# Kernel optimization log

Hardware: AMD Instinct MI355X
Metric: run time of the kernel (lower is better)

The kernel has to match this reference:

```python
import jax, jax.numpy as jnp
import numpy as np

DICTSIZE = 256
NUMCHAR = 1024
EMB_LEN = 512
KQV_LEN = 512
BATCH = 128


def setup_inputs() -> dict:
    key = jax.random.key(0)
    ks = jax.random.split(key, 7)
    input_tokens = jax.random.randint(ks[0], (BATCH, NUMCHAR), 0, DICTSIZE, dtype=jnp.int32)
    tok_emb = jax.random.normal(ks[1], (DICTSIZE, EMB_LEN), dtype=jnp.float32)
    Wq = jax.random.normal(ks[2], (KQV_LEN, EMB_LEN), dtype=jnp.float32) * (EMB_LEN ** -0.5)
    Wk = jax.random.normal(ks[3], (KQV_LEN, EMB_LEN), dtype=jnp.float32) * (EMB_LEN ** -0.5)
    Wv = jax.random.normal(ks[4], (KQV_LEN, EMB_LEN), dtype=jnp.float32) * (EMB_LEN ** -0.5)
    W_lin = jax.random.normal(ks[5], (DICTSIZE, NUMCHAR * EMB_LEN), dtype=jnp.float32) * ((NUMCHAR * EMB_LEN) ** -0.5)
    b_lin = jax.random.normal(ks[6], (DICTSIZE,), dtype=jnp.float32) * 0.01
    return {"input_tokens": input_tokens, "tok_emb": tok_emb, "Wq": Wq, "Wk": Wk,
            "Wv": Wv, "W_lin": W_lin, "b_lin": b_lin}


def reference(input_tokens, tok_emb, Wq, Wk, Wv, W_lin, b_lin):
    B, N = input_tokens.shape
    emb = tok_emb[input_tokens]                      # [B, N, E]
    q = jnp.einsum('bne,ke->bnk', emb, Wq)           # [B, N, K]
    k = jnp.einsum('bne,ke->bnk', emb, Wk)           # [B, N, K]
    v = jnp.einsum('bne,ke->bnk', emb, Wv)           # computed but unused (matches torch source)
    scores = jnp.einsum('bqk,bmk->bqm', q, k)        # [B, N, N] (no 1/sqrt(d) scaling in source)
    tril = jnp.tril(jnp.ones((N, N), dtype=bool))
    scores = jnp.where(tril, scores, -jnp.inf)
    attn = jax.nn.softmax(scores, axis=-1)           # [B, N, N]
    aff = jnp.einsum('bqm,bme->bqe', attn, emb)      # note: @ input_emb, NOT value
    aff_flat = aff.reshape(B, N * emb.shape[-1])     # [B, N*E]
    outputs = aff_flat @ W_lin.T + b_lin             # [B, dictsize]
    return outputs
```

## Files before the change

### kernel.cpp

```cpp
#include <hip/hip_runtime.h>

typedef _Float16 f16;
typedef _Float16 half8 __attribute__((ext_vector_type(8)));
typedef _Float16 half4 __attribute__((ext_vector_type(4)));
typedef float floatx4 __attribute__((ext_vector_type(4)));
typedef float floatx16 __attribute__((ext_vector_type(16)));

#define MFMA16(A, B, C) __builtin_amdgcn_mfma_f32_16x16x32_f16((A), (B), (C), 0, 0, 0)
#define MFMA32(A, B, C) __builtin_amdgcn_mfma_f32_32x32x16_f16((A), (B), (C), 0, 0, 0)


__global__ __launch_bounds__(256) void k_gemm_M(const float* __restrict__ Wq,
                                                const float* __restrict__ Wk,
                                                f16* __restrict__ Mt) {
  __shared__ __align__(16) float qa[16][64];
  __shared__ __align__(16) float kbs[16][64];
  const int tid = threadIdx.x;
  const int i0 = (blockIdx.x & 7) * 64;
  const int j0 = (blockIdx.x >> 3) * 64;
  const int tx = tid & 15, ty = tid >> 4;
  float acc[4][4] = {};
  for (int k0 = 0; k0 < 512; k0 += 16) {
    __syncthreads();
    const int kr = tid >> 4;
    const int c4 = (tid & 15) * 4;
    *(float4*)&qa[kr][c4]  = *(const float4*)&Wq[(k0 + kr) * 512 + i0 + c4];
    *(float4*)&kbs[kr][c4] = *(const float4*)&Wk[(k0 + kr) * 512 + j0 + c4];
    __syncthreads();
#pragma unroll
    for (int kk = 0; kk < 16; kk++) {
      float a[4], b[4];
#pragma unroll
      for (int x = 0; x < 4; x++) a[x] = qa[kk][ty * 4 + x];
#pragma unroll
      for (int y = 0; y < 4; y++) b[y] = kbs[kk][tx * 4 + y];
#pragma unroll
      for (int x = 0; x < 4; x++)
#pragma unroll
        for (int y = 0; y < 4; y++) acc[x][y] += a[x] * b[y];
    }
  }
#pragma unroll
  for (int x = 0; x < 4; x++)
#pragma unroll
    for (int y = 0; y < 4; y++)
      Mt[(j0 + tx * 4 + y) * 512 + (i0 + ty * 4 + x)] = (f16)acc[x][y];
}

__global__ __launch_bounds__(256) void k_gather(const int* __restrict__ tok,
                                                const float* __restrict__ temb,
                                                f16* __restrict__ embh) {
  const long g = (long)blockIdx.x * 256 + threadIdx.x;
  const long flat = g * 8;
  const int row = (int)(flat >> 9);
  const int e0 = (int)(flat & 511);
  const int t = tok[row];
  const float4 v0 = *(const float4*)&temb[t * 512 + e0];
  const float4 v1 = *(const float4*)&temb[t * 512 + e0 + 4];
  half8 h;
  h[0] = (f16)v0.x; h[1] = (f16)v0.y; h[2] = (f16)v0.z; h[3] = (f16)v0.w;
  h[4] = (f16)v1.x; h[5] = (f16)v1.y; h[6] = (f16)v1.z; h[7] = (f16)v1.w;
  *(half8*)&embh[flat] = h;
}

__global__ __launch_bounds__(256) void k_gatherT(const int* __restrict__ tok,
                                                 const float* __restrict__ temb,
                                                 f16* __restrict__ embt) {
  __shared__ int tl[64];
  const int b = blockIdx.y;
  const int n0 = (blockIdx.x & 15) * 64;
  const int e0 = (blockIdx.x >> 4) * 128;
  const int tid = threadIdx.x;
  if (tid < 64) tl[tid] = tok[b * 1024 + n0 + tid];
  __syncthreads();
  const int n8 = (tid & 7) * 8;
  const int e4 = e0 + (tid >> 3) * 4;
  float4 v[8];
#pragma unroll
  for (int j = 0; j < 8; j++) v[j] = *(const float4*)&temb[tl[n8 + j] * 512 + e4];
#pragma unroll
  for (int a = 0; a < 4; a++) {
    half8 h;
#pragma unroll
    for (int j = 0; j < 8; j++) h[j] = (f16)((&v[j].x)[a]);
    *(half8*)&embt[(((long)(b * 512 + e4 + a)) << 10) + n0 + n8] = h;
  }
}

__global__ __launch_bounds__(256) void k_gemm_T(const f16* __restrict__ A,
                                                const f16* __restrict__ Bt,
                                                f16* __restrict__ T) {
  __shared__ __align__(16) f16 smem[17408];
  f16* As = smem;
  f16* Bs = smem + 5120;
  const int tid = threadIdx.x;
  const long m0 = (long)blockIdx.y * 128;
  const int n0 = blockIdx.x * 128;
  const int w = tid >> 6, lane = tid & 63, lq = lane & 15, quad = lane >> 4;
  const int wm = w >> 1, wn = w & 1;
  floatx4 acc[4][4] = {};
  const int sr = tid >> 1, shc = (tid & 1) * 16;
  for (int k0 = 0; k0 < 512; k0 += 32) {
    half8 a0 = *(const half8*)&A[(m0 + sr) * 512 + k0 + shc];
    half8 a1 = *(const half8*)&A[(m0 + sr) * 512 + k0 + shc + 8];
    half8 b0 = *(const half8*)&Bt[(long)(n0 + sr) * 512 + k0 + shc];
    half8 b1 = *(const half8*)&Bt[(long)(n0 + sr) * 512 + k0 + shc + 8];
    __syncthreads();
    *(half8*)&As[sr * 40 + shc] = a0;
    *(half8*)&As[sr * 40 + shc + 8] = a1;
    *(half8*)&Bs[sr * 40 + shc] = b0;
    *(half8*)&Bs[sr * 40 + shc + 8] = b1;
    __syncthreads();
    half8 af[4], bf[4];
#pragma unroll
    for (int mt = 0; mt < 4; mt++) af[mt] = *(half8*)&As[(wm * 64 + mt * 16 + lq) * 40 + quad * 8];
#pragma unroll
    for (int nt = 0; nt < 4; nt++) bf[nt] = *(half8*)&Bs[(wn * 64 + nt * 16 + lq) * 40 + quad * 8];
#pragma unroll
    for (int mt = 0; mt < 4; mt++)
#pragma unroll
      for (int nt = 0; nt < 4; nt++) acc[mt][nt] = MFMA16(af[mt], bf[nt], acc[mt][nt]);
  }
  __syncthreads();
  f16* Cp = smem;
#pragma unroll
  for (int mt = 0; mt < 4; mt++)
#pragma unroll
    for (int nt = 0; nt < 4; nt++)
#pragma unroll
      for (int rr = 0; rr < 4; rr++)
        Cp[(wm * 64 + mt * 16 + quad * 4 + rr) * 136 + wn * 64 + nt * 16 + lq] =
            (f16)acc[mt][nt][rr];
  __syncthreads();
  const int orow = tid >> 1, occ = (tid & 1) * 64;
#pragma unroll
  for (int i = 0; i < 8; i++) {
    half8 hv = *(half8*)&Cp[orow * 136 + occ + i * 8];
    *(half8*)&T[(m0 + orow) * 512 + n0 + occ + i * 8] = hv;
  }
}

__global__ __launch_bounds__(256, 2) void k_attn3(const f16* __restrict__ embh,
                                                  const f16* __restrict__ embt,
                                                  f16* tq_aff) {
  __shared__ __align__(16) f16 smem[37888];
  __shared__ __align__(16) float wmax[4][32];
  __shared__ __align__(16) float wsum[4][32];
  __shared__ __align__(16) float alpha_s[64];
  __shared__ __align__(16) float l_s[64];
  f16* Qs = smem;
  f16* Pl = smem + 32768;

  const int tid = threadIdx.x;
  const int w = tid >> 6, lane = tid & 63;
  const int l31 = lane & 31, lh = lane >> 5;
  const int mh = w & 1, nh = w >> 1;

  const int bid = blockIdx.x;
  const int xcd = bid & 7, idx = bid >> 3;
  const int b = xcd * 16 + (idx >> 3);
  const int pair = idx & 7;
  const long bOff = (long)b * 1024 * 512;

  const int qrow = nh * 32 + l31;

  for (int t = 0; t < 2; t++) {
    const int qb = t ? (15 - pair) : pair;
    const int q0 = qb * 64;
    __syncthreads();
    {
      const int row = tid & 63, qo = tid >> 6;
      const f16* src = &tq_aff[bOff + (long)(q0 + row) * 512];
#pragma unroll
      for (int i = 0; i < 16; i++) {
        int g = qo * 16 + i;
        int gs = (g & ~7) | ((g ^ row) & 7);
        *(half8*)&Qs[row * 512 + gs * 8] = *(const half8*)&src[g * 8];
      }
    }
    __syncthreads();

    floatx16 Oa[2][4];
#pragma unroll
    for (int mt = 0; mt < 2; mt++)
#pragma unroll
      for (int nt = 0; nt < 4; nt++) Oa[mt][nt] = (floatx16)(0.f);
    float mrow = -1e30f, lrow = 0.f;
    const int qcol = q0 + nh * 32 + l31;

    for (int kb = 0; kb <= qb; kb++) {
      const f16* kptr = &embh[bOff + (long)(kb * 64 + mh * 32 + l31) * 512 + lh * 8];
      floatx16 st = {};
#pragma unroll
      for (int kc8 = 0; kc8 < 4; kc8++) {
        half8 a[8], bq[8];
#pragma unroll
        for (int i = 0; i < 8; i++) {
          const int kc = kc8 * 8 + i;
          a[i] = *(const half8*)&kptr[kc * 16];
          const int g = kc * 2 + lh;
          const int gs = (g & ~7) | ((g ^ qrow) & 7);
          bq[i] = *(half8*)&Qs[qrow * 512 + gs * 8];
        }
#pragma unroll
        for (int i = 0; i < 8; i++) st = MFMA32(a[i], bq[i], st);
      }
      float sv[16];
      float pm = -1e30f;
#pragma unroll
      for (int r = 0; r < 16; r++) {
        int keyr = kb * 64 + mh * 32 + (r & 3) + 8 * (r >> 2) + 4 * lh;
        float s = st[r];
        if (keyr > qcol) s = -1e30f;
        sv[r] = s;
        pm = fmaxf(pm, s);
      }
      pm = fmaxf(pm, __shfl_xor(pm, 32, 64));
      if (lane < 32) wmax[w][lane] = pm;
      __syncthreads();
      const float tmax = fmaxf(wmax[nh * 2][l31], wmax[nh * 2 + 1][l31]);
      const float mnew = fmaxf(mrow, tmax);
      const float al = exp2f((mrow - mnew) * 1.44269504f);
      float psum = 0.f;
      f16 ph[16];
#pragma unroll
      for (int r = 0; r < 16; r++) {
        float p = exp2f((sv[r] - mnew) * 1.44269504f);
        psum += p;
        ph[r] = (f16)p;
      }
      psum += __shfl_xor(psum, 32, 64);
      if (lane < 32) wsum[w][lane] = psum;
      if (mh == 0 && lane < 32) alpha_s[nh * 32 + lane] = al;
#pragma unroll
      for (int grp = 0; grp < 4; grp++) {
        half4 hp = {ph[grp * 4 + 0], ph[grp * 4 + 1], ph[grp * 4 + 2], ph[grp * 4 + 3]};
        *(half4*)&Pl[(nh * 32 + l31) * 72 + mh * 32 + grp * 8 + lh * 4] = hp;
      }
      mrow = mnew;
      __syncthreads();
      lrow = lrow * al + wsum[nh * 2][l31] + wsum[nh * 2 + 1][l31];
#pragma unroll
      for (int mt = 0; mt < 2; mt++)
#pragma unroll
        for (int grp = 0; grp < 4; grp++) {
          floatx4 av = *(floatx4*)&alpha_s[mt * 32 + grp * 8 + lh * 4];
#pragma unroll
          for (int nt = 0; nt < 4; nt++)
#pragma unroll
            for (int j = 0; j < 4; j++) Oa[mt][nt][grp * 4 + j] *= av[j];
        }
#pragma unroll
      for (int kc = 0; kc < 4; kc++) {
        half8 ap0 = *(half8*)&Pl[l31 * 72 + kc * 16 + lh * 8];
        half8 ap1 = *(half8*)&Pl[(32 + l31) * 72 + kc * 16 + lh * 8];
#pragma unroll
        for (int nt = 0; nt < 4; nt++) {
          const int e = w * 128 + nt * 32 + l31;
          half8 bv = *(const half8*)&embt[((long)(b * 512 + e) << 10) + kb * 64 +
                                          kc * 16 + lh * 8];
          Oa[0][nt] = MFMA32(ap0, bv, Oa[0][nt]);
          Oa[1][nt] = MFMA32(ap1, bv, Oa[1][nt]);
        }
      }
    }
    if (mh == 0 && lane < 32) l_s[nh * 32 + lane] = lrow;
    __syncthreads();
    f16* Ob = smem;
#pragma unroll
    for (int mt = 0; mt < 2; mt++)
#pragma unroll
      for (int grp = 0; grp < 4; grp++) {
        floatx4 lv = *(floatx4*)&l_s[mt * 32 + grp * 8 + lh * 4];
#pragma unroll
        for (int nt = 0; nt < 4; nt++) {
          const int col = w * 128 + nt * 32 + l31;
#pragma unroll
          for (int j = 0; j < 4; j++) {
            const int row = mt * 32 + grp * 8 + lh * 4 + j;
            Ob[row * 520 + col] = (f16)(Oa[mt][nt][grp * 4 + j] / lv[j]);
          }
        }
      }
    __syncthreads();
    {
      const int row = tid >> 2, seg = tid & 3;
#pragma unroll
      for (int i = 0; i < 16; i++) {
        half8 v = *(half8*)&Ob[row * 520 + seg * 128 + i * 8];
        *(half8*)&tq_aff[bOff + (long)(q0 + row) * 512 + seg * 128 + i * 8] = v;
      }
    }
  }
}

__global__ __launch_bounds__(256) void k_out_partial(const f16* __restrict__ aff,
                                                     const float* __restrict__ Wl,
                                                     float* __restrict__ part) {
  __shared__ __align__(16) f16 smem[15360];
  f16* As = smem;
  f16* Bs = smem + 5120;
  const int tid = threadIdx.x;
  const int w = tid >> 6, lane = tid & 63, lq = lane & 15, quad = lane >> 4;
  const int wm = w >> 1, wn = w & 1;
  const long kbase = (long)blockIdx.x * 1024;
  floatx4 acc[4][8] = {};
  const int rA = tid >> 1, hcA = (tid & 1) * 16;
  const int rB = tid >> 3, cB = (tid & 7) * 4;
  for (int k0 = 0; k0 < 1024; k0 += 32) {
    const long kk = kbase + k0;
    half8 a0 = *(const half8*)&aff[(long)rA * 524288 + kk + hcA];
    half8 a1 = *(const half8*)&aff[(long)rA * 524288 + kk + hcA + 8];
    float4 bv[8];
#pragma unroll
    for (int pass = 0; pass < 8; pass++)
      bv[pass] = *(const float4*)&Wl[(long)(pass * 32 + rB) * 524288 + kk + cB];
    __syncthreads();
    *(half8*)&As[rA * 40 + hcA] = a0;
    *(half8*)&As[rA * 40 + hcA + 8] = a1;
#pragma unroll
    for (int pass = 0; pass < 8; pass++) {
      half4 hb = {(f16)bv[pass].x, (f16)bv[pass].y, (f16)bv[pass].z, (f16)bv[pass].w};
      *(half4*)&Bs[(pass * 32 + rB) * 40 + cB] = hb;
    }
    __syncthreads();
    half8 af[4], bf[8];
#pragma unroll
    for (int mt = 0; mt < 4; mt++) af[mt] = *(half8*)&As[(wm * 64 + mt * 16 + lq) * 40 + quad * 8];
#pragma unroll
    for (int nt = 0; nt < 8; nt++) bf[nt] = *(half8*)&Bs[(wn * 128 + nt * 16 + lq) * 40 + quad * 8];
#pragma unroll
    for (int mt = 0; mt < 4; mt++)
#pragma unroll
      for (int nt = 0; nt < 8; nt++) acc[mt][nt] = MFMA16(af[mt], bf[nt], acc[mt][nt]);
  }
  float* po = part + (long)blockIdx.x * 32768;
#pragma unroll
  for (int mt = 0; mt < 4; mt++)
#pragma unroll
    for (int nt = 0; nt < 8; nt++)
#pragma unroll
      for (int rr = 0; rr < 4; rr++)
        po[(wm * 64 + mt * 16 + quad * 4 + rr) * 256 + wn * 128 + nt * 16 + lq] =
            acc[mt][nt][rr];
}

__global__ __launch_bounds__(256) void k_reduce(const float* __restrict__ part,
                                                const float* __restrict__ bl,
                                                float* __restrict__ out) {
  const int idx = blockIdx.x * 256 + threadIdx.x;
  float s = bl[idx & 255];
  for (int p = 0; p < 512; p++) s += part[(long)p * 32768 + idx];
  out[idx] = s;
}

extern "C" void kernel_launch(void* const* d_in, const int* in_sizes, int n_in,
                              void* d_out, int out_size, void* d_ws, size_t ws_size,
                              hipStream_t stream) {
  (void)in_sizes; (void)n_in; (void)out_size; (void)ws_size;
  const int* tok = (const int*)d_in[0];
  const float* temb = (const float*)d_in[1];
  const float* Wq = (const float*)d_in[2];
  const float* Wk = (const float*)d_in[3];
  const float* Wl = (const float*)d_in[5];
  const float* bl = (const float*)d_in[6];
  float* out = (float*)d_out;
  char* ws = (char*)d_ws;

  f16* embh = (f16*)(ws);
  f16* embt = (f16*)(ws + 134217728L);
  f16* Tq = (f16*)(ws + 268435456L);
  f16* Mt = (f16*)(ws + 402653184L);
  float* part = (float*)(ws);

  hipLaunchKernelGGL(k_gemm_M, dim3(64), dim3(256), 0, stream, Wq, Wk, Mt);
  hipLaunchKernelGGL(k_gather, dim3(32768), dim3(256), 0, stream, tok, temb, embh);
  hipLaunchKernelGGL(k_gatherT, dim3(64, 128), dim3(256), 0, stream, tok, temb, embt);
  hipLaunchKernelGGL(k_gemm_T, dim3(4, 1024), dim3(256), 0, stream, embh, Mt, Tq);
  hipLaunchKernelGGL(k_attn3, dim3(1024), dim3(256), 0, stream, embh, embt, Tq);
  hipLaunchKernelGGL(k_out_partial, dim3(512), dim3(256), 0, stream, Tq, Wl, part);
  hipLaunchKernelGGL(k_reduce, dim3(128), dim3(256), 0, stream, part, bl, out);
}
```

Measured before the change: 1.596 ms.

## Widen attention kernel to 8 waves with 128-key tiles and register prefetch

The causal attention kernel now runs 512 threads (8 waves) per block. Each step processes 128 keys instead of 64, which halves the number of key iterations and their block-wide barriers. Each wave now owns 64 output embedding columns instead of 128. K and V fragment loads from global memory are software-prefetched into registers one step ahead, so memory latency overlaps the MFMA work. In exchange, more masked work is wasted on diagonal tiles, the LDS footprint grows, and register pressure at 512 threads with 2 blocks per CU may limit occupancy.

```diff
diff --git a/kernel.cpp b/kernel.cpp
--- a/kernel.cpp
+++ b/kernel.cpp
@@ -140,12 +140,12 @@
   }
 }
 
-__global__ __launch_bounds__(256, 2) void k_attn3(const f16* __restrict__ embh,
+__global__ __launch_bounds__(512, 2) void k_attn4(const f16* __restrict__ embh,
                                                   const f16* __restrict__ embt,
                                                   f16* tq_aff) {
-  __shared__ __align__(16) f16 smem[37888];
-  __shared__ __align__(16) float wmax[4][32];
-  __shared__ __align__(16) float wsum[4][32];
+  __shared__ __align__(16) f16 smem[41472];
+  __shared__ __align__(16) float wmax[8][32];
+  __shared__ __align__(16) float wsum[8][32];
   __shared__ __align__(16) float alpha_s[64];
   __shared__ __align__(16) float l_s[64];
   f16* Qs = smem;
@@ -154,7 +154,7 @@
   const int tid = threadIdx.x;
   const int w = tid >> 6, lane = tid & 63;
   const int l31 = lane & 31, lh = lane >> 5;
-  const int mh = w & 1, nh = w >> 1;
+  const int mh = w & 3, nh = w >> 2;
 
   const int bid = blockIdx.x;
   const int xcd = bid & 7, idx = bid >> 3;
@@ -169,47 +169,57 @@
     const int q0 = qb * 64;
     __syncthreads();
     {
-      const int row = tid & 63, qo = tid >> 6;
+      const int row = tid >> 3;
+      const int c0 = (tid & 7) * 8;
       const f16* src = &tq_aff[bOff + (long)(q0 + row) * 512];
 #pragma unroll
-      for (int i = 0; i < 16; i++) {
-        int g = qo * 16 + i;
+      for (int i = 0; i < 8; i++) {
+        int g = c0 + i;
         int gs = (g & ~7) | ((g ^ row) & 7);
         *(half8*)&Qs[row * 512 + gs * 8] = *(const half8*)&src[g * 8];
       }
     }
     __syncthreads();
 
-    floatx16 Oa[2][4];
+    floatx16 Oa[2][2];
 #pragma unroll
     for (int mt = 0; mt < 2; mt++)
 #pragma unroll
-      for (int nt = 0; nt < 4; nt++) Oa[mt][nt] = (floatx16)(0.f);
+      for (int nt = 0; nt < 2; nt++) Oa[mt][nt] = (floatx16)(0.f);
     float mrow = -1e30f, lrow = 0.f;
     const int qcol = q0 + nh * 32 + l31;
-
-    for (int kb = 0; kb <= qb; kb++) {
-      const f16* kptr = &embh[bOff + (long)(kb * 64 + mh * 32 + l31) * 512 + lh * 8];
+    const int nkb = (qb + 2) >> 1;
+
+    for (int kb = 0; kb < nkb; kb++) {
+      const f16* kptr = &embh[bOff + (long)(kb * 128 + mh * 32 + l31) * 512 + lh * 8];
       floatx16 st = {};
-#pragma unroll
-      for (int kc8 = 0; kc8 < 4; kc8++) {
-        half8 a[8], bq[8];
+      half8 a_cur[8], a_nxt[8];
+#pragma unroll
+      for (int i = 0; i < 8; i++) a_cur[i] = *(const half8*)&kptr[i * 16];
+#pragma unroll
+      for (int r = 0; r < 4; r++) {
+        if (r < 3) {
+#pragma unroll
+          for (int i = 0; i < 8; i++) a_nxt[i] = *(const half8*)&kptr[(r * 8 + 8 + i) * 16];
+        }
 #pragma unroll
         for (int i = 0; i < 8; i++) {
-          const int kc = kc8 * 8 + i;
-          a[i] = *(const half8*)&kptr[kc * 16];
+          const int kc = r * 8 + i;
           const int g = kc * 2 + lh;
           const int gs = (g & ~7) | ((g ^ qrow) & 7);
-          bq[i] = *(half8*)&Qs[qrow * 512 + gs * 8];
-        }
-#pragma unroll
-        for (int i = 0; i < 8; i++) st = MFMA32(a[i], bq[i], st);
+          half8 bq = *(half8*)&Qs[qrow * 512 + gs * 8];
+          st = MFMA32(a_cur[i], bq, st);
+        }
+        if (r < 3) {
+#pragma unroll
+          for (int i = 0; i < 8; i++) a_cur[i] = a_nxt[i];
+        }
       }
       float sv[16];
       float pm = -1e30f;
 #pragma unroll
       for (int r = 0; r < 16; r++) {
-        int keyr = kb * 64 + mh * 32 + (r & 3) + 8 * (r >> 2) + 4 * lh;
+        int keyr = kb * 128 + mh * 32 + (r & 3) + 8 * (r >> 2) + 4 * lh;
         float s = st[r];
         if (keyr > qcol) s = -1e30f;
         sv[r] = s;
@@ -218,7 +228,8 @@
       pm = fmaxf(pm, __shfl_xor(pm, 32, 64));
       if (lane < 32) wmax[w][lane] = pm;
       __syncthreads();
-      const float tmax = fmaxf(wmax[nh * 2][l31], wmax[nh * 2 + 1][l31]);
+      const float tmax = fmaxf(fmaxf(wmax[nh * 4 + 0][l31], wmax[nh * 4 + 1][l31]),
+                               fmaxf(wmax[nh * 4 + 2][l31], wmax[nh * 4 + 3][l31]));
       const float mnew = fmaxf(mrow, tmax);
       const float al = exp2f((mrow - mnew) * 1.44269504f);
       float psum = 0.f;
@@ -235,32 +246,45 @@
 #pragma unroll
       for (int grp = 0; grp < 4; grp++) {
         half4 hp = {ph[grp * 4 + 0], ph[grp * 4 + 1], ph[grp * 4 + 2], ph[grp * 4 + 3]};
-        *(half4*)&Pl[(nh * 32 + l31) * 72 + mh * 32 + grp * 8 + lh * 4] = hp;
+        *(half4*)&Pl[(nh * 32 + l31) * 136 + mh * 32 + grp * 8 + lh * 4] = hp;
       }
       mrow = mnew;
       __syncthreads();
-      lrow = lrow * al + wsum[nh * 2][l31] + wsum[nh * 2 + 1][l31];
+      lrow = lrow * al + wsum[nh * 4 + 0][l31] + wsum[nh * 4 + 1][l31] +
+             wsum[nh * 4 + 2][l31] + wsum[nh * 4 + 3][l31];
 #pragma unroll
       for (int mt = 0; mt < 2; mt++)
 #pragma unroll
         for (int grp = 0; grp < 4; grp++) {
           floatx4 av = *(floatx4*)&alpha_s[mt * 32 + grp * 8 + lh * 4];
 #pragma unroll
-          for (int nt = 0; nt < 4; nt++)
+          for (int nt = 0; nt < 2; nt++)
 #pragma unroll
             for (int j = 0; j < 4; j++) Oa[mt][nt][grp * 4 + j] *= av[j];
         }
-#pragma unroll
-      for (int kc = 0; kc < 4; kc++) {
-        half8 ap0 = *(half8*)&Pl[l31 * 72 + kc * 16 + lh * 8];
-        half8 ap1 = *(half8*)&Pl[(32 + l31) * 72 + kc * 16 + lh * 8];
-#pragma unroll
-        for (int nt = 0; nt < 4; nt++) {
-          const int e = w * 128 + nt * 32 + l31;
-          half8 bv = *(const half8*)&embt[((long)(b * 512 + e) << 10) + kb * 64 +
-                                          kc * 16 + lh * 8];
-          Oa[0][nt] = MFMA32(ap0, bv, Oa[0][nt]);
-          Oa[1][nt] = MFMA32(ap1, bv, Oa[1][nt]);
+      const f16* vbase = &embt[((long)(b * 512 + w * 64) << 10) + kb * 128];
+      half8 bv0[2], bv1[2];
+#pragma unroll
+      for (int nt = 0; nt < 2; nt++)
+        bv0[nt] = *(const half8*)&vbase[((long)(nt * 32 + l31) << 10) + lh * 8];
+#pragma unroll
+      for (int kq = 0; kq < 8; kq++) {
+        if (kq < 7) {
+#pragma unroll
+          for (int nt = 0; nt < 2; nt++)
+            bv1[nt] = *(const half8*)&vbase[((long)(nt * 32 + l31) << 10) +
+                                            (kq + 1) * 16 + lh * 8];
+        }
+        half8 ap0 = *(half8*)&Pl[l31 * 136 + kq * 16 + lh * 8];
+        half8 ap1 = *(half8*)&Pl[(32 + l31) * 136 + kq * 16 + lh * 8];
+#pragma unroll
+        for (int nt = 0; nt < 2; nt++) {
+          Oa[0][nt] = MFMA32(ap0, bv0[nt], Oa[0][nt]);
+          Oa[1][nt] = MFMA32(ap1, bv0[nt], Oa[1][nt]);
+        }
+        if (kq < 7) {
+#pragma unroll
+          for (int nt = 0; nt < 2; nt++) bv0[nt] = bv1[nt];
         }
       }
     }
@@ -273,8 +297,8 @@
       for (int grp = 0; grp < 4; grp++) {
         floatx4 lv = *(floatx4*)&l_s[mt * 32 + grp * 8 + lh * 4];
 #pragma unroll
-        for (int nt = 0; nt < 4; nt++) {
-          const int col = w * 128 + nt * 32 + l31;
+        for (int nt = 0; nt < 2; nt++) {
+          const int col = w * 64 + nt * 32 + l31;
 #pragma unroll
           for (int j = 0; j < 4; j++) {
             const int row = mt * 32 + grp * 8 + lh * 4 + j;
@@ -284,11 +308,11 @@
       }
     __syncthreads();
     {
-      const int row = tid >> 2, seg = tid & 3;
-#pragma unroll
-      for (int i = 0; i < 16; i++) {
-        half8 v = *(half8*)&Ob[row * 520 + seg * 128 + i * 8];
-        *(half8*)&tq_aff[bOff + (long)(q0 + row) * 512 + seg * 128 + i * 8] = v;
+      const int row = tid >> 3, c0 = (tid & 7) * 64;
+#pragma unroll
+      for (int i = 0; i < 8; i++) {
+        half8 v = *(half8*)&Ob[row * 520 + c0 + i * 8];
+        *(half8*)&tq_aff[bOff + (long)(q0 + row) * 512 + c0 + i * 8] = v;
       }
     }
   }
@@ -377,7 +401,7 @@
   hipLaunchKernelGGL(k_gather, dim3(32768), dim3(256), 0, stream, tok, temb, embh);
   hipLaunchKernelGGL(k_gatherT, dim3(64, 128), dim3(256), 0, stream, tok, temb, embt);
   hipLaunchKernelGGL(k_gemm_T, dim3(4, 1024), dim3(256), 0, stream, embh, Mt, Tq);
-  hipLaunchKernelGGL(k_attn3, dim3(1024), dim3(256), 0, stream, embh, embt, Tq);
+  hipLaunchKernelGGL(k_attn4, dim3(1024), dim3(512), 0, stream, embh, embt, Tq);
   hipLaunchKernelGGL(k_out_partial, dim3(512), dim3(256), 0, stream, Tq, Wl, part);
   hipLaunchKernelGGL(k_reduce, dim3(128), dim3(256), 0, stream, part, bl, out);
 }
```

Result: no change. 1.616 ms (+1.3%).

## Warp-specialize attention with LDS double-buffered K tiles and transposed LDS reads

Applied to the files above, without the earlier changes.

Rewrites the attention kernel with 512 threads. Four producer waves stream the next key tile into a double-buffered LDS area using global_load_lds, while four consumer waves compute QK^T with Q held in registers. The P·V step reads the same LDS tile through ds_read_b64_tr_b16 transposed reads, so the separate transposed-embedding gather kernel and its global buffer are removed. This cuts global traffic and overlaps loads with compute, but uses much more LDS and registers (which can lower occupancy) and adds extra barriers.

```diff
diff --git a/kernel.cpp b/kernel.cpp
--- a/kernel.cpp
+++ b/kernel.cpp
@@ -8,6 +8,22 @@
 
 #define MFMA16(A, B, C) __builtin_amdgcn_mfma_f32_16x16x32_f16((A), (B), (C), 0, 0, 0)
 #define MFMA32(A, B, C) __builtin_amdgcn_mfma_f32_32x32x16_f16((A), (B), (C), 0, 0, 0)
+
+#define GLDS16(src, dst)                                      \
+  __builtin_amdgcn_global_load_lds(                           \
+      (const __attribute__((address_space(1))) void*)(src),   \
+      (__attribute__((address_space(3))) void*)(dst), 16, 0, 0)
+
+#define TR_READ(dstv, p)                                        \
+  asm volatile("ds_read_b64_tr_b16 %0, %1"                      \
+               : "=v"(dstv)                                     \
+               : "v"((__attribute__((address_space(3))) f16*)(p)))
+
+#define BARRIER_LGKM()                                        \
+  do {                                                        \
+    asm volatile("s_waitcnt lgkmcnt(0)" ::: "memory");        \
+    __builtin_amdgcn_s_barrier();                             \
+  } while (0)
 
 
 __global__ __launch_bounds__(256) void k_gemm_M(const float* __restrict__ Wq,
@@ -61,30 +77,6 @@
   h[0] = (f16)v0.x; h[1] = (f16)v0.y; h[2] = (f16)v0.z; h[3] = (f16)v0.w;
   h[4] = (f16)v1.x; h[5] = (f16)v1.y; h[6] = (f16)v1.z; h[7] = (f16)v1.w;
   *(half8*)&embh[flat] = h;
-}
-
-__global__ __launch_bounds__(256) void k_gatherT(const int* __restrict__ tok,
-                                                 const float* __restrict__ temb,
-                                                 f16* __restrict__ embt) {
-  __shared__ int tl[64];
-  const int b = blockIdx.y;
-  const int n0 = (blockIdx.x & 15) * 64;
-  const int e0 = (blockIdx.x >> 4) * 128;
-  const int tid = threadIdx.x;
-  if (tid < 64) tl[tid] = tok[b * 1024 + n0 + tid];
-  __syncthreads();
-  const int n8 = (tid & 7) * 8;
-  const int e4 = e0 + (tid >> 3) * 4;
-  float4 v[8];
-#pragma unroll
-  for (int j = 0; j < 8; j++) v[j] = *(const float4*)&temb[tl[n8 + j] * 512 + e4];
-#pragma unroll
-  for (int a = 0; a < 4; a++) {
-    half8 h;
-#pragma unroll
-    for (int j = 0; j < 8; j++) h[j] = (f16)((&v[j].x)[a]);
-    *(half8*)&embt[(((long)(b * 512 + e4 + a)) << 10) + n0 + n8] = h;
-  }
 }
 
 __global__ __launch_bounds__(256) void k_gemm_T(const f16* __restrict__ A,
@@ -140,21 +132,19 @@
   }
 }
 
-__global__ __launch_bounds__(256, 2) void k_attn3(const f16* __restrict__ embh,
-                                                  const f16* __restrict__ embt,
+__global__ __launch_bounds__(512, 2) void k_attn5(const f16* __restrict__ embh,
                                                   f16* tq_aff) {
-  __shared__ __align__(16) f16 smem[37888];
+  __shared__ __align__(16) f16 Kl[2][32768];
+  __shared__ __align__(16) f16 Pl[64 * 72];
   __shared__ __align__(16) float wmax[4][32];
   __shared__ __align__(16) float wsum[4][32];
   __shared__ __align__(16) float alpha_s[64];
   __shared__ __align__(16) float l_s[64];
-  f16* Qs = smem;
-  f16* Pl = smem + 32768;
 
   const int tid = threadIdx.x;
   const int w = tid >> 6, lane = tid & 63;
   const int l31 = lane & 31, lh = lane >> 5;
-  const int mh = w & 1, nh = w >> 1;
+  const int lq = lane & 15, quad = lane >> 4;
 
   const int bid = blockIdx.x;
   const int xcd = bid & 7, idx = bid >> 3;
@@ -162,133 +152,173 @@
   const int pair = idx & 7;
   const long bOff = (long)b * 1024 * 512;
 
-  const int qrow = nh * 32 + l31;
+  const int mh = w & 1, nh = w >> 1;
+  const int qrow_l = nh * 32 + l31;
+
+  const int kqi = l31 >> 2;
+  const int p8i = (kqi >> 1) | ((kqi & 1) << 2);
+  const int abase_off = mh * 512 + p8i * 64 + (l31 & 3) * 16 + lh * 8;
+  const int trbase_off = (w * 4) * 1024 + lane * 4;
 
   for (int t = 0; t < 2; t++) {
     const int qb = t ? (15 - pair) : pair;
     const int q0 = qb * 64;
     __syncthreads();
+
+#pragma unroll
+    for (int i = 0; i < 8; i++) {
+      const int cbase = (w * 8 + i) * 64;
+      const int c = cbase + lane;
+      const int es = c >> 7, ks2 = (c >> 6) & 1, sp8 = (c >> 3) & 7,
+                kr = (c >> 1) & 3, el8 = c & 1;
+      const int skq = ((sp8 & 3) << 1) | (sp8 >> 2);
+      const int k = ks2 * 32 + skq * 4 + kr;
+      const int e = es * 16 + el8 * 8;
+      GLDS16(&embh[bOff + (long)k * 512 + e], &Kl[0][cbase * 8]);
+    }
+    half8 qreg[32];
+    if (w < 4) {
+      const f16* qsrc = &tq_aff[bOff + (long)(q0 + qrow_l) * 512 + lh * 8];
+#pragma unroll
+      for (int kc = 0; kc < 32; kc++) qreg[kc] = *(const half8*)&qsrc[kc * 16];
+    }
+    floatx4 Oa[4][4];
+#pragma unroll
+    for (int mt = 0; mt < 4; mt++)
+#pragma unroll
+      for (int nt = 0; nt < 4; nt++) Oa[mt][nt] = (floatx4)(0.f);
+    float mrow = -1e30f, lrow = 0.f;
+    const int qcol = q0 + qrow_l;
+
+    asm volatile("s_waitcnt vmcnt(0)" ::: "memory");
+    __builtin_amdgcn_s_barrier();
+    int cur = 0;
+    const int nkb = qb + 1;
+
+    for (int kb = 0; kb < nkb; kb++) {
+      float sv[16];
+      if (w >= 4) {
+        if (kb < qb) {
+          const int nxt = cur ^ 1;
+#pragma unroll
+          for (int i = 0; i < 16; i++) {
+            const int cbase = ((w - 4) * 16 + i) * 64;
+            const int c = cbase + lane;
+            const int es = c >> 7, ks2 = (c >> 6) & 1, sp8 = (c >> 3) & 7,
+                      kr = (c >> 1) & 3, el8 = c & 1;
+            const int skq = ((sp8 & 3) << 1) | (sp8 >> 2);
+            const int k = ks2 * 32 + skq * 4 + kr;
+            const int e = es * 16 + el8 * 8;
+            GLDS16(&embh[bOff + (long)((kb + 1) * 64 + k) * 512 + e],
+                   &Kl[nxt][cbase * 8]);
+          }
+        }
+      } else {
+        const f16* ab = &Kl[cur][abase_off];
+        floatx16 st = {};
+#pragma unroll
+        for (int kc8 = 0; kc8 < 4; kc8++) {
+          half8 a[8];
+#pragma unroll
+          for (int i = 0; i < 8; i++) a[i] = *(const half8*)&ab[(kc8 * 8 + i) * 1024];
+#pragma unroll
+          for (int i = 0; i < 8; i++) st = MFMA32(a[i], qreg[kc8 * 8 + i], st);
+        }
+        float pm = -1e30f;
+#pragma unroll
+        for (int r = 0; r < 16; r++) {
+          const int keyr = kb * 64 + mh * 32 + (r & 3) + 8 * (r >> 2) + 4 * lh;
+          float s = st[r];
+          if (keyr > qcol) s = -1e30f;
+          sv[r] = s;
+          pm = fmaxf(pm, s);
+        }
+        pm = fmaxf(pm, __shfl_xor(pm, 32, 64));
+        if (lane < 32) wmax[w][lane] = pm;
+      }
+      BARRIER_LGKM();
+      float al = 0.f;
+      if (w < 4) {
+        const float tmax = fmaxf(wmax[nh * 2][l31], wmax[nh * 2 + 1][l31]);
+        const float mnew = fmaxf(mrow, tmax);
+        al = exp2f((mrow - mnew) * 1.44269504f);
+        float psum = 0.f;
+        f16 ph[16];
+#pragma unroll
+        for (int r = 0; r < 16; r++) {
+          const float p = exp2f((sv[r] - mnew) * 1.44269504f);
+          psum += p;
+          ph[r] = (f16)p;
+        }
+        psum += __shfl_xor(psum, 32, 64);
+        if (lane < 32) wsum[w][lane] = psum;
+        if (mh == 0 && lane < 32) alpha_s[nh * 32 + lane] = al;
+#pragma unroll
+        for (int grp = 0; grp < 4; grp++) {
+          half4 hp = {ph[grp * 4 + 0], ph[grp * 4 + 1], ph[grp * 4 + 2], ph[grp * 4 + 3]};
+          *(half4*)&Pl[(nh * 32 + l31) * 72 + mh * 32 + grp * 8 + lh * 4] = hp;
+        }
+        mrow = mnew;
+      }
+      BARRIER_LGKM();
+      if (w < 4) lrow = lrow * al + wsum[nh * 2][l31] + wsum[nh * 2 + 1][l31];
+#pragma unroll
+      for (int mt = 0; mt < 4; mt++) {
+        const floatx4 av = *(const floatx4*)&alpha_s[mt * 16 + quad * 4];
+#pragma unroll
+        for (int nt = 0; nt < 4; nt++)
+#pragma unroll
+          for (int rr = 0; rr < 4; rr++) Oa[mt][nt][rr] *= av[rr];
+      }
+#pragma unroll
+      for (int ksv = 0; ksv < 2; ksv++) {
+        f16* trp = &Kl[cur][trbase_off + ksv * 512];
+        half4 t0[4], t1[4];
+#pragma unroll
+        for (int nt = 0; nt < 4; nt++) {
+          TR_READ(t0[nt], trp + nt * 1024);
+          TR_READ(t1[nt], trp + nt * 1024 + 256);
+        }
+        half8 ap[4];
+#pragma unroll
+        for (int mt = 0; mt < 4; mt++)
+          ap[mt] = *(const half8*)&Pl[(mt * 16 + lq) * 72 + ksv * 32 + quad * 8];
+        asm volatile("s_waitcnt lgkmcnt(0)" ::: "memory");
+        __builtin_amdgcn_sched_barrier(0);
+        half8 bv[4];
+#pragma unroll
+        for (int nt = 0; nt < 4; nt++)
+          bv[nt] = __builtin_shufflevector(t0[nt], t1[nt], 0, 1, 2, 3, 4, 5, 6, 7);
+#pragma unroll
+        for (int mt = 0; mt < 4; mt++)
+#pragma unroll
+          for (int nt = 0; nt < 4; nt++) Oa[mt][nt] = MFMA16(ap[mt], bv[nt], Oa[mt][nt]);
+      }
+      if (w >= 4) asm volatile("s_waitcnt vmcnt(0)" ::: "memory");
+      BARRIER_LGKM();
+      cur ^= 1;
+    }
+    if (w < 4 && mh == 0 && lane < 32) l_s[nh * 32 + lane] = lrow;
+    __syncthreads();
+    f16* Ob = &Kl[0][0];
+#pragma unroll
+    for (int mt = 0; mt < 4; mt++) {
+      const floatx4 lv = *(const floatx4*)&l_s[mt * 16 + quad * 4];
+#pragma unroll
+      for (int nt = 0; nt < 4; nt++) {
+        const int col = w * 64 + nt * 16 + lq;
+#pragma unroll
+        for (int rr = 0; rr < 4; rr++)
+          Ob[(mt * 16 + quad * 4 + rr) * 520 + col] = (f16)(Oa[mt][nt][rr] / lv[rr]);
+      }
+    }
+    __syncthreads();
     {
-      const int row = tid & 63, qo = tid >> 6;
-      const f16* src = &tq_aff[bOff + (long)(q0 + row) * 512];
-#pragma unroll
-      for (int i = 0; i < 16; i++) {
-        int g = qo * 16 + i;
-        int gs = (g & ~7) | ((g ^ row) & 7);
-        *(half8*)&Qs[row * 512 + gs * 8] = *(const half8*)&src[g * 8];
-      }
-    }
-    __syncthreads();
-
-    floatx16 Oa[2][4];
-#pragma unroll
-    for (int mt = 0; mt < 2; mt++)
-#pragma unroll
-      for (int nt = 0; nt < 4; nt++) Oa[mt][nt] = (floatx16)(0.f);
-    float mrow = -1e30f, lrow = 0.f;
-    const int qcol = q0 + nh * 32 + l31;
-
-    for (int kb = 0; kb <= qb; kb++) {
-      const f16* kptr = &embh[bOff + (long)(kb * 64 + mh * 32 + l31) * 512 + lh * 8];
-      floatx16 st = {};
-#pragma unroll
-      for (int kc8 = 0; kc8 < 4; kc8++) {
-        half8 a[8], bq[8];
-#pragma unroll
-        for (int i = 0; i < 8; i++) {
-          const int kc = kc8 * 8 + i;
-          a[i] = *(const half8*)&kptr[kc * 16];
-          const int g = kc * 2 + lh;
-          const int gs = (g & ~7) | ((g ^ qrow) & 7);
-          bq[i] = *(half8*)&Qs[qrow * 512 + gs * 8];
-        }
-#pragma unroll
-        for (int i = 0; i < 8; i++) st = MFMA32(a[i], bq[i], st);
-      }
-      float sv[16];
-      float pm = -1e30f;
-#pragma unroll
-      for (int r = 0; r < 16; r++) {
-        int keyr = kb * 64 + mh * 32 + (r & 3) + 8 * (r >> 2) + 4 * lh;
-        float s = st[r];
-        if (keyr > qcol) s = -1e30f;
-        sv[r] = s;
-        pm = fmaxf(pm, s);
-      }
-      pm = fmaxf(pm, __shfl_xor(pm, 32, 64));
-      if (lane < 32) wmax[w][lane] = pm;
-      __syncthreads();
-      const float tmax = fmaxf(wmax[nh * 2][l31], wmax[nh * 2 + 1][l31]);
-      const float mnew = fmaxf(mrow, tmax);
-      const float al = exp2f((mrow - mnew) * 1.44269504f);
-      float psum = 0.f;
-      f16 ph[16];
-#pragma unroll
-      for (int r = 0; r < 16; r++) {
-        float p = exp2f((sv[r] - mnew) * 1.44269504f);
-        psum += p;
-        ph[r] = (f16)p;
-      }
-      psum += __shfl_xor(psum, 32, 64);
-      if (lane < 32) wsum[w][lane] = psum;
-      if (mh == 0 && lane < 32) alpha_s[nh * 32 + lane] = al;
-#pragma unroll
-      for (int grp = 0; grp < 4; grp++) {
-        half4 hp = {ph[grp * 4 + 0], ph[grp * 4 + 1], ph[grp * 4 + 2], ph[grp * 4 + 3]};
-        *(half4*)&Pl[(nh * 32 + l31) * 72 + mh * 32 + grp * 8 + lh * 4] = hp;
-      }
-      mrow = mnew;
-      __syncthreads();
-      lrow = lrow * al + wsum[nh * 2][l31] + wsum[nh * 2 + 1][l31];
-#pragma unroll
-      for (int mt = 0; mt < 2; mt++)
-#pragma unroll
-        for (int grp = 0; grp < 4; grp++) {
-          floatx4 av = *(floatx4*)&alpha_s[mt * 32 + grp * 8 + lh * 4];
-#pragma unroll
-          for (int nt = 0; nt < 4; nt++)
-#pragma unroll
-            for (int j = 0; j < 4; j++) Oa[mt][nt][grp * 4 + j] *= av[j];
-        }
-#pragma unroll
-      for (int kc = 0; kc < 4; kc++) {
-        half8 ap0 = *(half8*)&Pl[l31 * 72 + kc * 16 + lh * 8];
-        half8 ap1 = *(half8*)&Pl[(32 + l31) * 72 + kc * 16 + lh * 8];
-#pragma unroll
-        for (int nt = 0; nt < 4; nt++) {
-          const int e = w * 128 + nt * 32 + l31;
-          half8 bv = *(const half8*)&embt[((long)(b * 512 + e) << 10) + kb * 64 +
-                                          kc * 16 + lh * 8];
-          Oa[0][nt] = MFMA32(ap0, bv, Oa[0][nt]);
-          Oa[1][nt] = MFMA32(ap1, bv, Oa[1][nt]);
-        }
-      }
-    }
-    if (mh == 0 && lane < 32) l_s[nh * 32 + lane] = lrow;
-    __syncthreads();
-    f16* Ob = smem;
-#pragma unroll
-    for (int mt = 0; mt < 2; mt++)
-#pragma unroll
-      for (int grp = 0; grp < 4; grp++) {
-        floatx4 lv = *(floatx4*)&l_s[mt * 32 + grp * 8 + lh * 4];
-#pragma unroll
-        for (int nt = 0; nt < 4; nt++) {
-          const int col = w * 128 + nt * 32 + l31;
-#pragma unroll
-          for (int j = 0; j < 4; j++) {
-            const int row = mt * 32 + grp * 8 + lh * 4 + j;
-            Ob[row * 520 + col] = (f16)(Oa[mt][nt][grp * 4 + j] / lv[j]);
-          }
-        }
-      }
-    __syncthreads();
-    {
-      const int row = tid >> 2, seg = tid & 3;
-#pragma unroll
-      for (int i = 0; i < 16; i++) {
-        half8 v = *(half8*)&Ob[row * 520 + seg * 128 + i * 8];
-        *(half8*)&tq_aff[bOff + (long)(q0 + row) * 512 + seg * 128 + i * 8] = v;
+      const int row = tid >> 3, c0 = (tid & 7) * 64;
+#pragma unroll
+      for (int i = 0; i < 8; i++) {
+        half8 v = *(half8*)&Ob[row * 520 + c0 + i * 8];
+        *(half8*)&tq_aff[bOff + (long)(q0 + row) * 512 + c0 + i * 8] = v;
       }
     }
   }
@@ -368,16 +398,14 @@
   char* ws = (char*)d_ws;
 
   f16* embh = (f16*)(ws);
-  f16* embt = (f16*)(ws + 134217728L);
   f16* Tq = (f16*)(ws + 268435456L);
   f16* Mt = (f16*)(ws + 402653184L);
   float* part = (float*)(ws);
 
   hipLaunchKernelGGL(k_gemm_M, dim3(64), dim3(256), 0, stream, Wq, Wk, Mt);
   hipLaunchKernelGGL(k_gather, dim3(32768), dim3(256), 0, stream, tok, temb, embh);
-  hipLaunchKernelGGL(k_gatherT, dim3(64, 128), dim3(256), 0, stream, tok, temb, embt);
   hipLaunchKernelGGL(k_gemm_T, dim3(4, 1024), dim3(256), 0, stream, embh, Mt, Tq);
-  hipLaunchKernelGGL(k_attn3, dim3(1024), dim3(256), 0, stream, embh, embt, Tq);
+  hipLaunchKernelGGL(k_attn5, dim3(1024), dim3(512), 0, stream, embh, Tq);
   hipLaunchKernelGGL(k_out_partial, dim3(512), dim3(256), 0, stream, Tq, Wl, part);
   hipLaunchKernelGGL(k_reduce, dim3(128), dim3(256), 0, stream, part, bl, out);
 }
```

Result: slower. 1.657 ms (+3.8%).
